# Kernel tuning notes

Hardware: AMD Instinct MI355X
Metric: run time of the kernel (lower is better)

The kernel has to match this reference:

```python
import jax, jax.numpy as jnp
import numpy as np

B, N, H, E, M = 2, 20000, 256, 160000, 512


def setup_inputs() -> dict:
    key = jax.random.key(0)
    ks = jax.random.split(key, 8)
    s = 0.02  # small init scale like trained nets
    return {
        "h": jax.random.normal(ks[0], (B, N, H), jnp.float32),
        "edge_index": jax.random.randint(ks[1], (2, E), 0, N, jnp.int64),
        "msg_w1": jax.random.normal(ks[2], (2 * H, M), jnp.float32) * s,
        "msg_b1": jnp.zeros((M,), jnp.float32),
        "msg_w2": jax.random.normal(ks[3], (M, H), jnp.float32) * s,
        "msg_b2": jnp.zeros((H,), jnp.float32),
        "upd_w1": jax.random.normal(ks[4], (2 * H, M), jnp.float32) * s,
        "upd_b1": jnp.zeros((M,), jnp.float32),
        "upd_w2": jax.random.normal(ks[5], (M, H), jnp.float32) * s,
        "upd_b2": jnp.zeros((H,), jnp.float32),
    }


def _mlp(x, w1, b1, w2, b2):
    return jax.nn.relu(x @ w1 + b1) @ w2 + b2


def reference(h, edge_index, msg_w1, msg_b1, msg_w2, msg_b2,
              upd_w1, upd_b1, upd_w2, upd_b2):
    src, dst = edge_index[0], edge_index[1]
    h_src = h[:, src, :]                         # [B,E,H] gather
    h_dst = h[:, dst, :]                         # [B,E,H] gather
    m = _mlp(jnp.concatenate([h_src, h_dst], axis=-1),
             msg_w1, msg_b1, msg_w2, msg_b2)     # [B,E,H]
    agg = jnp.zeros_like(h).at[:, dst, :].add(m) # scatter-add over dst
    upd = _mlp(jnp.concatenate([h, agg], axis=-1),
               upd_w1, upd_b1, upd_w2, upd_b2)   # [B,N,H]
    return h + upd  # mp_residual=True
```

## Files before the change

### kernel.cpp

```cpp
#include <hip/hip_runtime.h>
#include <hip/hip_bf16.h>
#include <stdint.h>

#define B_ 2
#define N_ 20000
#define H_ 256
#define E_ 160000
#define M_ 512

typedef short bf16x8 __attribute__((ext_vector_type(8)));
typedef float f32x4 __attribute__((ext_vector_type(4)));

__device__ __forceinline__ unsigned short f2bf(float f) {
    union { float f; unsigned u; } cv; cv.f = f;
    unsigned u = cv.u;
    unsigned r = u + 0x7fffu + ((u >> 16) & 1u);
    return (unsigned short)(r >> 16);
}
__device__ __forceinline__ unsigned pack2(float a, float b) {
    return (unsigned)f2bf(a) | ((unsigned)f2bf(b) << 16);
}
__device__ __forceinline__ float bflo(unsigned p) {
    union { unsigned u; float f; } c; c.u = p << 16; return c.f;
}
__device__ __forceinline__ float bfhi(unsigned p) {
    union { unsigned u; float f; } c; c.u = p & 0xffff0000u; return c.f;
}

__global__ void conv_t(const float* __restrict__ W, unsigned short* __restrict__ Wt,
                       int K, int Ncol) {
    int total = Ncol * (K >> 3);
    for (int idx = blockIdx.x * blockDim.x + threadIdx.x; idx < total;
         idx += gridDim.x * blockDim.x) {
        int n = idx % Ncol;
        int kc = (idx / Ncol) << 3;
        unsigned short t[8];
#pragma unroll
        for (int j = 0; j < 8; ++j) t[j] = f2bf(W[(size_t)(kc + j) * Ncol + n]);
        uint4 v;
        v.x = (unsigned)t[0] | ((unsigned)t[1] << 16);
        v.y = (unsigned)t[2] | ((unsigned)t[3] << 16);
        v.z = (unsigned)t[4] | ((unsigned)t[5] << 16);
        v.w = (unsigned)t[6] | ((unsigned)t[7] << 16);
        *(uint4*)(Wt + (size_t)n * K + kc) = v;
    }
}

__global__ void conv_w1pq(const float* __restrict__ W, unsigned short* __restrict__ Wt) {
    int total = 1024 * 32;
    for (int idx = blockIdx.x * blockDim.x + threadIdx.x; idx < total;
         idx += gridDim.x * blockDim.x) {
        int jj = idx & 1023;
        int kc = (idx >> 10) << 3;
        int koff = (jj >= 512) ? 256 : 0;
        int j = jj & 511;
        unsigned short t[8];
#pragma unroll
        for (int r = 0; r < 8; ++r) t[r] = f2bf(W[(size_t)(kc + r + koff) * 512 + j]);
        uint4 v;
        v.x = (unsigned)t[0] | ((unsigned)t[1] << 16);
        v.y = (unsigned)t[2] | ((unsigned)t[3] << 16);
        v.z = (unsigned)t[4] | ((unsigned)t[5] << 16);
        v.w = (unsigned)t[6] | ((unsigned)t[7] << 16);
        *(uint4*)(Wt + (size_t)jj * 256 + kc) = v;
    }
}

__global__ void hist_kernel(const int* __restrict__ eidx, int* __restrict__ cnt) {
    for (int e = blockIdx.x * blockDim.x + threadIdx.x; e < E_;
         e += gridDim.x * blockDim.x)
        atomicAdd(cnt + eidx[E_ + e], 1);
}

__global__ void scan_kernel(const int* __restrict__ cnt, int* __restrict__ offs,
                            int* __restrict__ cursor) {
    __shared__ int part[1024];
    int t = threadIdx.x;
    int base_i = t * 20;
    int loc[20];
    int s = 0;
#pragma unroll 20
    for (int i = 0; i < 20; ++i) {
        int idx = base_i + i;
        int v = (idx < N_) ? cnt[idx] : 0;
        loc[i] = s;
        s += v;
    }
    part[t] = s;
    __syncthreads();
    for (int off = 1; off < 1024; off <<= 1) {
        int tmp = (t >= off) ? part[t - off] : 0;
        __syncthreads();
        if (t >= off) part[t] += tmp;
        __syncthreads();
    }
    int base = part[t] - s;
#pragma unroll 20
    for (int i = 0; i < 20; ++i) {
        int idx = base_i + i;
        if (idx < N_) {
            int o = base + loc[i];
            offs[idx] = o;
            cursor[idx] = o;
        }
    }
    if (t == 1023) offs[N_] = part[1023];
}

__global__ void scatter_kernel(const int* __restrict__ eidx, int* __restrict__ cursor,
                               int* __restrict__ sorted) {
    for (int e = blockIdx.x * blockDim.x + threadIdx.x; e < E_;
         e += gridDim.x * blockDim.x) {
        int d = eidx[E_ + e];
        int pos = atomicAdd(cursor + d, 1);
        sorted[pos] = e;
    }
}

__global__ __launch_bounds__(512, 4) void pq_gemm(
    const float* __restrict__ hb,
    const unsigned short* __restrict__ W1pq,
    unsigned short* __restrict__ PQ) {
    __shared__ char smem[32 * 512];
    const int tid = threadIdx.x;
    const int row0 = blockIdx.x * 32;

#pragma unroll
    for (int it = 0; it < 4; ++it) {
        int linear = it * 512 + tid;
        int row = linear >> 6;
        int c4 = linear & 63;
        float4 v = *(const float4*)(hb + (size_t)(row0 + row) * H_ + c4 * 4);
        int byte = (row * 512 + c4 * 8) ^ ((row & 7) << 4);
        uint2 p;
        p.x = pack2(v.x, v.y);
        p.y = pack2(v.z, v.w);
        *(uint2*)(smem + byte) = p;
    }
    __syncthreads();

    const int lane = tid & 63;
    const int w = tid >> 6;
    const int lo = lane & 15;
    const int hi = lane >> 4;

    f32x4 acc[2][8];
#pragma unroll
    for (int i = 0; i < 2; ++i)
#pragma unroll
        for (int j = 0; j < 8; ++j) acc[i][j] = (f32x4){0.f, 0.f, 0.f, 0.f};

    for (int ks = 0; ks < 256; ks += 32) {
        bf16x8 af[2];
#pragma unroll
        for (int rf = 0; rf < 2; ++rf) {
            int row = rf * 16 + lo;
            int byte = (row * 512 + (ks + 8 * hi) * 2) ^ ((row & 7) << 4);
            af[rf] = *(const bf16x8*)(smem + byte);
        }
#pragma unroll
        for (int cf = 0; cf < 8; ++cf) {
            int col = w * 128 + cf * 16 + lo;
            bf16x8 bfr = *(const bf16x8*)(W1pq + (size_t)col * 256 + ks + 8 * hi);
#pragma unroll
            for (int rf = 0; rf < 2; ++rf)
                acc[rf][cf] = __builtin_amdgcn_mfma_f32_16x16x32_bf16(af[rf], bfr, acc[rf][cf], 0, 0, 0);
        }
    }

#pragma unroll
    for (int cf = 0; cf < 8; ++cf) {
        int col = w * 128 + cf * 16 + lo;
#pragma unroll
        for (int rf = 0; rf < 2; ++rf) {
#pragma unroll
            for (int r = 0; r < 4; ++r) {
                int row = rf * 16 + hi * 4 + r;
                PQ[(size_t)(row0 + row) * 1024 + col] = f2bf(acc[rf][cf][r]);
            }
        }
    }
}

__global__ __launch_bounds__(512, 4) void agg_kernel(
    const unsigned short* __restrict__ PQ,
    const int* __restrict__ eidx,
    const int* __restrict__ sorted,
    const int* __restrict__ offs,
    const int* __restrict__ cnt,
    const unsigned short* __restrict__ w2t,
    const float* __restrict__ b1,
    const float* __restrict__ b2,
    unsigned short* __restrict__ aggb) {
    __shared__ char smem[32 * 1024];
    const int tid = threadIdx.x;
    const int d0 = blockIdx.x * 32;
    const int dsub = tid >> 4;
    const int part = tid & 15;
    const int c0 = part * 32;
    const int d = d0 + dsub;

    unsigned qb[16];
    {
        const unsigned short* qrow = PQ + (size_t)d * 1024 + 512 + c0;
#pragma unroll
        for (int c = 0; c < 4; ++c) {
            bf16x8 qv = *(const bf16x8*)(qrow + c * 8);
#pragma unroll
            for (int jp = 0; jp < 4; ++jp) {
                float q0 = bflo((unsigned)(unsigned short)qv[jp * 2]) + b1[c0 + c * 8 + jp * 2];
                float q1 = bflo((unsigned)(unsigned short)qv[jp * 2 + 1]) + b1[c0 + c * 8 + jp * 2 + 1];
                qb[c * 4 + jp] = pack2(q0, q1);
            }
        }
    }

    float acc[32];
#pragma unroll
    for (int i = 0; i < 32; ++i) acc[i] = 0.f;

    const int beg = offs[d];
    const int end = beg + cnt[d];
    for (int p = beg; p < end; ++p) {
        int e = sorted[p];
        int src = eidx[e];
        const unsigned short* prow = PQ + (size_t)src * 1024 + c0;
#pragma unroll
        for (int c = 0; c < 4; ++c) {
            bf16x8 pv = *(const bf16x8*)(prow + c * 8);
#pragma unroll
            for (int jp = 0; jp < 4; ++jp) {
                unsigned q = qb[c * 4 + jp];
                float p0 = bflo((unsigned)(unsigned short)pv[jp * 2]);
                float p1 = bflo((unsigned)(unsigned short)pv[jp * 2 + 1]);
                acc[c * 8 + jp * 2]     += fmaxf(p0 + bflo(q), 0.f);
                acc[c * 8 + jp * 2 + 1] += fmaxf(p1 + bfhi(q), 0.f);
            }
        }
    }

#pragma unroll
    for (int c = 0; c < 4; ++c) {
        uint4 v;
        v.x = pack2(acc[c * 8 + 0], acc[c * 8 + 1]);
        v.y = pack2(acc[c * 8 + 2], acc[c * 8 + 3]);
        v.z = pack2(acc[c * 8 + 4], acc[c * 8 + 5]);
        v.w = pack2(acc[c * 8 + 6], acc[c * 8 + 7]);
        int byte = (dsub * 1024 + (c0 + c * 8) * 2) ^ ((dsub & 7) << 4);
        *(uint4*)(smem + byte) = v;
    }
    __syncthreads();

    const int lane = tid & 63;
    const int w = tid >> 6;
    const int lo = lane & 15;
    const int hi = lane >> 4;

    f32x4 acc2[2][2];
#pragma unroll
    for (int i = 0; i < 2; ++i)
#pragma unroll
        for (int j = 0; j < 2; ++j) acc2[i][j] = (f32x4){0.f, 0.f, 0.f, 0.f};

    for (int ks = 0; ks < 512; ks += 32) {
        bf16x8 af[2];
#pragma unroll
        for (int rf = 0; rf < 2; ++rf) {
            int row = rf * 16 + lo;
            int byte = (row * 1024 + (ks + 8 * hi) * 2) ^ ((row & 7) << 4);
            af[rf] = *(const bf16x8*)(smem + byte);
        }
#pragma unroll
        for (int cf = 0; cf < 2; ++cf) {
            int col = w * 32 + cf * 16 + lo;
            bf16x8 bfr = *(const bf16x8*)(w2t + (size_t)col * 512 + ks + 8 * hi);
#pragma unroll
            for (int rf = 0; rf < 2; ++rf)
                acc2[rf][cf] = __builtin_amdgcn_mfma_f32_16x16x32_bf16(af[rf], bfr, acc2[rf][cf], 0, 0, 0);
        }
    }

#pragma unroll
    for (int cf = 0; cf < 2; ++cf) {
        int col = w * 32 + cf * 16 + lo;
        float bb = b2[col];
#pragma unroll
        for (int rf = 0; rf < 2; ++rf) {
#pragma unroll
            for (int r = 0; r < 4; ++r) {
                int row = rf * 16 + hi * 4 + r;
                float degf = (float)cnt[d0 + row];
                float v = acc2[rf][cf][r] + degf * bb;
                aggb[(size_t)(d0 + row) * 256 + col] = f2bf(v);
            }
        }
    }
}

__global__ __launch_bounds__(256, 4) void upd_kernel(
    const float* __restrict__ h,
    const unsigned short* __restrict__ aggb,
    const unsigned short* __restrict__ u1t,
    const float* __restrict__ b1,
    const unsigned short* __restrict__ u2t,
    const float* __restrict__ b2,
    float* __restrict__ outp) {
    __shared__ char smem[32 * 1024];
    const int tid = threadIdx.x;
    const int row0 = blockIdx.x * 32;

#pragma unroll
    for (int it = 0; it < 8; ++it) {
        int linear = it * 256 + tid;
        int row = linear >> 6;
        int c8 = linear & 63;
        int grow = row0 + row;
        uint4 v;
        if (c8 < 32) {
            const float* src = h + (size_t)grow * H_ + c8 * 8;
            float4 a = *(const float4*)src;
            float4 b = *(const float4*)(src + 4);
            v.x = pack2(a.x, a.y);
            v.y = pack2(a.z, a.w);
            v.z = pack2(b.x, b.y);
            v.w = pack2(b.z, b.w);
        } else {
            v = *(const uint4*)(aggb + (size_t)grow * 256 + (c8 - 32) * 8);
        }
        int byte = (row * 1024 + c8 * 16) ^ ((row & 7) << 4);
        *(uint4*)(smem + byte) = v;
    }
    __syncthreads();

    const int lane = tid & 63;
    const int w = tid >> 6;
    const int lo = lane & 15;
    const int hi = lane >> 4;

    f32x4 acc[2][8];
#pragma unroll
    for (int i = 0; i < 2; ++i)
#pragma unroll
        for (int j = 0; j < 8; ++j) acc[i][j] = (f32x4){0.f, 0.f, 0.f, 0.f};

    for (int ks = 0; ks < 512; ks += 32) {
        bf16x8 af[2];
#pragma unroll
        for (int rf = 0; rf < 2; ++rf) {
            int row = rf * 16 + lo;
            int byte = (row * 1024 + (ks + 8 * hi) * 2) ^ ((row & 7) << 4);
            af[rf] = *(const bf16x8*)(smem + byte);
        }
#pragma unroll
        for (int cf = 0; cf < 8; ++cf) {
            int col = w * 128 + cf * 16 + lo;
            bf16x8 bfr = *(const bf16x8*)(u1t + (size_t)col * 512 + ks + 8 * hi);
#pragma unroll
            for (int rf = 0; rf < 2; ++rf)
                acc[rf][cf] = __builtin_amdgcn_mfma_f32_16x16x32_bf16(af[rf], bfr, acc[rf][cf], 0, 0, 0);
        }
    }
    __syncthreads();

#pragma unroll
    for (int cf = 0; cf < 8; ++cf) {
        int col = w * 128 + cf * 16 + lo;
        float bb = b1[col];
#pragma unroll
        for (int rf = 0; rf < 2; ++rf) {
#pragma unroll
            for (int r = 0; r < 4; ++r) {
                float v = fmaxf(acc[rf][cf][r] + bb, 0.f);
                int row = rf * 16 + hi * 4 + r;
                int byte = (row * 1024 + col * 2) ^ ((row & 7) << 4);
                *(unsigned short*)(smem + byte) = f2bf(v);
            }
        }
    }
    __syncthreads();

    f32x4 acc2[2][4];
#pragma unroll
    for (int i = 0; i < 2; ++i)
#pragma unroll
        for (int j = 0; j < 4; ++j) acc2[i][j] = (f32x4){0.f, 0.f, 0.f, 0.f};

    for (int ks = 0; ks < 512; ks += 32) {
        bf16x8 af[2];
#pragma unroll
        for (int rf = 0; rf < 2; ++rf) {
            int row = rf * 16 + lo;
            int byte = (row * 1024 + (ks + 8 * hi) * 2) ^ ((row & 7) << 4);
            af[rf] = *(const bf16x8*)(smem + byte);
        }
#pragma unroll
        for (int cf = 0; cf < 4; ++cf) {
            int col = w * 64 + cf * 16 + lo;
            bf16x8 bfr = *(const bf16x8*)(u2t + (size_t)col * 512 + ks + 8 * hi);
#pragma unroll
            for (int rf = 0; rf < 2; ++rf)
                acc2[rf][cf] = __builtin_amdgcn_mfma_f32_16x16x32_bf16(af[rf], bfr, acc2[rf][cf], 0, 0, 0);
        }
    }

#pragma unroll
    for (int cf = 0; cf < 4; ++cf) {
        int col = w * 64 + cf * 16 + lo;
        float bb = b2[col];
#pragma unroll
        for (int rf = 0; rf < 2; ++rf) {
#pragma unroll
            for (int r = 0; r < 4; ++r) {
                int row = rf * 16 + hi * 4 + r;
                size_t o = (size_t)(row0 + row) * H_ + col;
                outp[o] = h[o] + acc2[rf][cf][r] + bb;
            }
        }
    }
}

extern "C" void kernel_launch(void* const* d_in, const int* in_sizes, int n_in,
                              void* d_out, int out_size, void* d_ws, size_t ws_size,
                              hipStream_t stream) {
    const float* h      = (const float*)d_in[0];
    const int*   eidx   = (const int*)d_in[1];
    const float* msg_w1 = (const float*)d_in[2];
    const float* msg_b1 = (const float*)d_in[3];
    const float* msg_w2 = (const float*)d_in[4];
    const float* msg_b2 = (const float*)d_in[5];
    const float* upd_w1 = (const float*)d_in[6];
    const float* upd_b1 = (const float*)d_in[7];
    const float* upd_w2 = (const float*)d_in[8];
    const float* upd_b2 = (const float*)d_in[9];
    float* out = (float*)d_out;

    char* ws = (char*)d_ws;
    size_t off = 0;
    auto alloc = [&](size_t bytes) {
        char* p = ws + off;
        off = (off + bytes + 255) & ~(size_t)255;
        return p;
    };
    unsigned short* PQ    = (unsigned short*)alloc((size_t)N_ * 1024 * 2);
    unsigned short* aggb  = (unsigned short*)alloc((size_t)B_ * N_ * 256 * 2);
    unsigned short* w1pq  = (unsigned short*)alloc(1024 * 256 * 2);
    unsigned short* w2t   = (unsigned short*)alloc(256 * 512 * 2);
    unsigned short* u1t   = (unsigned short*)alloc(512 * 512 * 2);
    unsigned short* u2t   = (unsigned short*)alloc(256 * 512 * 2);
    int* cnt    = (int*)alloc(N_ * 4);
    int* offs   = (int*)alloc((N_ + 1) * 4);
    int* cursor = (int*)alloc(N_ * 4);
    int* sorted = (int*)alloc(E_ * 4);
    if (ws_size < off) return;

    hipMemsetAsync(cnt, 0, N_ * 4, stream);
    conv_w1pq<<<64, 256, 0, stream>>>(msg_w1, w1pq);
    conv_t<<<64, 256, 0, stream>>>(msg_w2, w2t, 512, 256);
    conv_t<<<128, 256, 0, stream>>>(upd_w1, u1t, 512, 512);
    conv_t<<<64, 256, 0, stream>>>(upd_w2, u2t, 512, 256);

    hist_kernel<<<256, 256, 0, stream>>>(eidx, cnt);
    scan_kernel<<<1, 1024, 0, stream>>>(cnt, offs, cursor);
    scatter_kernel<<<256, 256, 0, stream>>>(eidx, cursor, sorted);

    for (int b = 0; b < B_; ++b) {
        pq_gemm<<<N_ / 32, 512, 0, stream>>>(h + (size_t)b * N_ * H_, w1pq, PQ);
        agg_kernel<<<N_ / 32, 512, 0, stream>>>(PQ, eidx, sorted, offs, cnt, w2t,
                                                msg_b1, msg_b2,
                                                aggb + (size_t)b * N_ * 256);
    }

    upd_kernel<<<(B_ * N_) / 32, 256, 0, stream>>>(h, aggb, u1t, upd_b1, u2t, upd_b2, out);
}
```

Before: 487.3 us.

## Enlarge GEMM tiles, prefetch weights, store src ids directly, interleave agg columns

Several changes land together. The four weight-conversion launches become one kernel, and the CSR array now stores source node ids so the agg loop skips one indirection. The agg loop handles two edges per iteration with an interleaved column layout so gather loads coalesce across lanes. The pq_gemm and upd_kernel tiles grow to 64 rows (upd now runs 512 threads), and all MFMA loops register-prefetch the next B fragment. Larger tiles and prefetch buffers raise register and LDS pressure and may lower occupancy.

```diff
diff --git a/kernel.cpp b/kernel.cpp
--- a/kernel.cpp
+++ b/kernel.cpp
@@ -27,42 +27,52 @@
     union { unsigned u; float f; } c; c.u = p & 0xffff0000u; return c.f;
 }
 
-__global__ void conv_t(const float* __restrict__ W, unsigned short* __restrict__ Wt,
-                       int K, int Ncol) {
-    int total = Ncol * (K >> 3);
-    for (int idx = blockIdx.x * blockDim.x + threadIdx.x; idx < total;
-         idx += gridDim.x * blockDim.x) {
-        int n = idx % Ncol;
-        int kc = (idx / Ncol) << 3;
-        unsigned short t[8];
-#pragma unroll
-        for (int j = 0; j < 8; ++j) t[j] = f2bf(W[(size_t)(kc + j) * Ncol + n]);
-        uint4 v;
-        v.x = (unsigned)t[0] | ((unsigned)t[1] << 16);
-        v.y = (unsigned)t[2] | ((unsigned)t[3] << 16);
-        v.z = (unsigned)t[4] | ((unsigned)t[5] << 16);
-        v.w = (unsigned)t[6] | ((unsigned)t[7] << 16);
-        *(uint4*)(Wt + (size_t)n * K + kc) = v;
-    }
-}
-
-__global__ void conv_w1pq(const float* __restrict__ W, unsigned short* __restrict__ Wt) {
-    int total = 1024 * 32;
-    for (int idx = blockIdx.x * blockDim.x + threadIdx.x; idx < total;
-         idx += gridDim.x * blockDim.x) {
-        int jj = idx & 1023;
-        int kc = (idx >> 10) << 3;
-        int koff = (jj >= 512) ? 256 : 0;
-        int j = jj & 511;
-        unsigned short t[8];
-#pragma unroll
-        for (int r = 0; r < 8; ++r) t[r] = f2bf(W[(size_t)(kc + r + koff) * 512 + j]);
-        uint4 v;
-        v.x = (unsigned)t[0] | ((unsigned)t[1] << 16);
-        v.y = (unsigned)t[2] | ((unsigned)t[3] << 16);
-        v.z = (unsigned)t[4] | ((unsigned)t[5] << 16);
-        v.w = (unsigned)t[6] | ((unsigned)t[7] << 16);
-        *(uint4*)(Wt + (size_t)jj * 256 + kc) = v;
+__device__ __forceinline__ void conv_t_one(const float* __restrict__ W,
+                                           unsigned short* __restrict__ Wt,
+                                           int K, int Ncol, int idx) {
+    int n = idx % Ncol;
+    int kc = (idx / Ncol) << 3;
+    unsigned short t[8];
+#pragma unroll
+    for (int j = 0; j < 8; ++j) t[j] = f2bf(W[(size_t)(kc + j) * Ncol + n]);
+    uint4 v;
+    v.x = (unsigned)t[0] | ((unsigned)t[1] << 16);
+    v.y = (unsigned)t[2] | ((unsigned)t[3] << 16);
+    v.z = (unsigned)t[4] | ((unsigned)t[5] << 16);
+    v.w = (unsigned)t[6] | ((unsigned)t[7] << 16);
+    *(uint4*)(Wt + (size_t)n * K + kc) = v;
+}
+
+__device__ __forceinline__ void conv_w1pq_one(const float* __restrict__ W,
+                                              unsigned short* __restrict__ Wt, int idx) {
+    int jj = idx & 1023;
+    int kc = (idx >> 10) << 3;
+    int koff = (jj >= 512) ? 256 : 0;
+    int j = jj & 511;
+    unsigned short t[8];
+#pragma unroll
+    for (int r = 0; r < 8; ++r) t[r] = f2bf(W[(size_t)(kc + r + koff) * 512 + j]);
+    uint4 v;
+    v.x = (unsigned)t[0] | ((unsigned)t[1] << 16);
+    v.y = (unsigned)t[2] | ((unsigned)t[3] << 16);
+    v.z = (unsigned)t[4] | ((unsigned)t[5] << 16);
+    v.w = (unsigned)t[6] | ((unsigned)t[7] << 16);
+    *(uint4*)(Wt + (size_t)jj * 256 + kc) = v;
+}
+
+__global__ void conv_all(const float* __restrict__ mw1, const float* __restrict__ mw2,
+                         const float* __restrict__ uw1, const float* __restrict__ uw2,
+                         unsigned short* __restrict__ w1pq, unsigned short* __restrict__ w2t,
+                         unsigned short* __restrict__ u1t, unsigned short* __restrict__ u2t) {
+    int idx = blockIdx.x * blockDim.x + threadIdx.x;
+    if (idx < 32768) {
+        conv_w1pq_one(mw1, w1pq, idx);
+    } else if (idx < 32768 + 16384) {
+        conv_t_one(mw2, w2t, 512, 256, idx - 32768);
+    } else if (idx < 32768 + 16384 + 32768) {
+        conv_t_one(uw1, u1t, 512, 512, idx - (32768 + 16384));
+    } else if (idx < 98304) {
+        conv_t_one(uw2, u2t, 512, 256, idx - (32768 + 16384 + 32768));
     }
 }
 
@@ -108,12 +118,12 @@
 }
 
 __global__ void scatter_kernel(const int* __restrict__ eidx, int* __restrict__ cursor,
-                               int* __restrict__ sorted) {
+                               int* __restrict__ srcs) {
     for (int e = blockIdx.x * blockDim.x + threadIdx.x; e < E_;
          e += gridDim.x * blockDim.x) {
         int d = eidx[E_ + e];
         int pos = atomicAdd(cursor + d, 1);
-        sorted[pos] = e;
+        srcs[pos] = eidx[e];
     }
 }
 
@@ -121,16 +131,18 @@
     const float* __restrict__ hb,
     const unsigned short* __restrict__ W1pq,
     unsigned short* __restrict__ PQ) {
-    __shared__ char smem[32 * 512];
+    __shared__ char smem[64 * 512];
     const int tid = threadIdx.x;
-    const int row0 = blockIdx.x * 32;
-
-#pragma unroll
-    for (int it = 0; it < 4; ++it) {
+    const int row0 = blockIdx.x * 64;
+
+#pragma unroll
+    for (int it = 0; it < 8; ++it) {
         int linear = it * 512 + tid;
         int row = linear >> 6;
         int c4 = linear & 63;
-        float4 v = *(const float4*)(hb + (size_t)(row0 + row) * H_ + c4 * 4);
+        int grow = row0 + row;
+        if (grow >= N_) grow = N_ - 1;
+        float4 v = *(const float4*)(hb + (size_t)grow * H_ + c4 * 4);
         int byte = (row * 512 + c4 * 8) ^ ((row & 7) << 4);
         uint2 p;
         p.x = pack2(v.x, v.y);
@@ -143,40 +155,55 @@
     const int w = tid >> 6;
     const int lo = lane & 15;
     const int hi = lane >> 4;
-
-    f32x4 acc[2][8];
-#pragma unroll
-    for (int i = 0; i < 2; ++i)
+    const int colw = w * 128;
+
+    f32x4 acc[4][8];
+#pragma unroll
+    for (int i = 0; i < 4; ++i)
 #pragma unroll
         for (int j = 0; j < 8; ++j) acc[i][j] = (f32x4){0.f, 0.f, 0.f, 0.f};
 
+    bf16x8 bcur[8];
+#pragma unroll
+    for (int cf = 0; cf < 8; ++cf)
+        bcur[cf] = *(const bf16x8*)(W1pq + (size_t)(colw + cf * 16 + lo) * 256 + 8 * hi);
+
+#pragma unroll
     for (int ks = 0; ks < 256; ks += 32) {
-        bf16x8 af[2];
-#pragma unroll
-        for (int rf = 0; rf < 2; ++rf) {
+        bf16x8 bnx[8];
+        if (ks + 32 < 256) {
+#pragma unroll
+            for (int cf = 0; cf < 8; ++cf)
+                bnx[cf] = *(const bf16x8*)(W1pq + (size_t)(colw + cf * 16 + lo) * 256 + ks + 32 + 8 * hi);
+        }
+        bf16x8 af[4];
+#pragma unroll
+        for (int rf = 0; rf < 4; ++rf) {
             int row = rf * 16 + lo;
             int byte = (row * 512 + (ks + 8 * hi) * 2) ^ ((row & 7) << 4);
             af[rf] = *(const bf16x8*)(smem + byte);
         }
 #pragma unroll
-        for (int cf = 0; cf < 8; ++cf) {
-            int col = w * 128 + cf * 16 + lo;
-            bf16x8 bfr = *(const bf16x8*)(W1pq + (size_t)col * 256 + ks + 8 * hi);
-#pragma unroll
-            for (int rf = 0; rf < 2; ++rf)
-                acc[rf][cf] = __builtin_amdgcn_mfma_f32_16x16x32_bf16(af[rf], bfr, acc[rf][cf], 0, 0, 0);
+        for (int cf = 0; cf < 8; ++cf)
+#pragma unroll
+            for (int rf = 0; rf < 4; ++rf)
+                acc[rf][cf] = __builtin_amdgcn_mfma_f32_16x16x32_bf16(af[rf], bcur[cf], acc[rf][cf], 0, 0, 0);
+        if (ks + 32 < 256) {
+#pragma unroll
+            for (int cf = 0; cf < 8; ++cf) bcur[cf] = bnx[cf];
         }
     }
 
 #pragma unroll
     for (int cf = 0; cf < 8; ++cf) {
-        int col = w * 128 + cf * 16 + lo;
-#pragma unroll
-        for (int rf = 0; rf < 2; ++rf) {
+        int col = colw + cf * 16 + lo;
+#pragma unroll
+        for (int rf = 0; rf < 4; ++rf) {
 #pragma unroll
             for (int r = 0; r < 4; ++r) {
                 int row = rf * 16 + hi * 4 + r;
-                PQ[(size_t)(row0 + row) * 1024 + col] = f2bf(acc[rf][cf][r]);
+                if (row0 + row < N_)
+                    PQ[(size_t)(row0 + row) * 1024 + col] = f2bf(acc[rf][cf][r]);
             }
         }
     }
@@ -184,8 +211,7 @@
 
 __global__ __launch_bounds__(512, 4) void agg_kernel(
     const unsigned short* __restrict__ PQ,
-    const int* __restrict__ eidx,
-    const int* __restrict__ sorted,
+    const int* __restrict__ srcs,
     const int* __restrict__ offs,
     const int* __restrict__ cnt,
     const unsigned short* __restrict__ w2t,
@@ -197,19 +223,19 @@
     const int d0 = blockIdx.x * 32;
     const int dsub = tid >> 4;
     const int part = tid & 15;
-    const int c0 = part * 32;
     const int d = d0 + dsub;
 
     unsigned qb[16];
     {
-        const unsigned short* qrow = PQ + (size_t)d * 1024 + 512 + c0;
+        const unsigned short* qrow = PQ + (size_t)d * 1024 + 512;
 #pragma unroll
         for (int c = 0; c < 4; ++c) {
-            bf16x8 qv = *(const bf16x8*)(qrow + c * 8);
+            int cb = (c * 16 + part) * 8;
+            bf16x8 qv = *(const bf16x8*)(qrow + cb);
 #pragma unroll
             for (int jp = 0; jp < 4; ++jp) {
-                float q0 = bflo((unsigned)(unsigned short)qv[jp * 2]) + b1[c0 + c * 8 + jp * 2];
-                float q1 = bflo((unsigned)(unsigned short)qv[jp * 2 + 1]) + b1[c0 + c * 8 + jp * 2 + 1];
+                float q0 = bflo((unsigned)(unsigned short)qv[jp * 2]) + b1[cb + jp * 2];
+                float q1 = bflo((unsigned)(unsigned short)qv[jp * 2 + 1]) + b1[cb + jp * 2 + 1];
                 qb[c * 4 + jp] = pack2(q0, q1);
             }
         }
@@ -220,21 +246,43 @@
     for (int i = 0; i < 32; ++i) acc[i] = 0.f;
 
     const int beg = offs[d];
-    const int end = beg + cnt[d];
-    for (int p = beg; p < end; ++p) {
-        int e = sorted[p];
-        int src = eidx[e];
-        const unsigned short* prow = PQ + (size_t)src * 1024 + c0;
+    const int end = offs[d + 1];
+    int p = beg;
+    for (; p + 1 < end; p += 2) {
+        int s0 = srcs[p];
+        int s1 = srcs[p + 1];
+        const unsigned short* r0 = PQ + (size_t)s0 * 1024;
+        const unsigned short* r1 = PQ + (size_t)s1 * 1024;
+        bf16x8 v0[4], v1[4];
 #pragma unroll
         for (int c = 0; c < 4; ++c) {
-            bf16x8 pv = *(const bf16x8*)(prow + c * 8);
+            v0[c] = *(const bf16x8*)(r0 + (c * 16 + part) * 8);
+            v1[c] = *(const bf16x8*)(r1 + (c * 16 + part) * 8);
+        }
+#pragma unroll
+        for (int c = 0; c < 4; ++c) {
 #pragma unroll
             for (int jp = 0; jp < 4; ++jp) {
                 unsigned q = qb[c * 4 + jp];
-                float p0 = bflo((unsigned)(unsigned short)pv[jp * 2]);
-                float p1 = bflo((unsigned)(unsigned short)pv[jp * 2 + 1]);
-                acc[c * 8 + jp * 2]     += fmaxf(p0 + bflo(q), 0.f);
-                acc[c * 8 + jp * 2 + 1] += fmaxf(p1 + bfhi(q), 0.f);
+                float ql = bflo(q), qh = bfhi(q);
+                acc[c * 8 + jp * 2] += fmaxf(bflo((unsigned)(unsigned short)v0[c][jp * 2]) + ql, 0.f)
+                                     + fmaxf(bflo((unsigned)(unsigned short)v1[c][jp * 2]) + ql, 0.f);
+                acc[c * 8 + jp * 2 + 1] += fmaxf(bflo((unsigned)(unsigned short)v0[c][jp * 2 + 1]) + qh, 0.f)
+                                         + fmaxf(bflo((unsigned)(unsigned short)v1[c][jp * 2 + 1]) + qh, 0.f);
+            }
+        }
+    }
+    if (p < end) {
+        int s0 = srcs[p];
+        const unsigned short* r0 = PQ + (size_t)s0 * 1024;
+#pragma unroll
+        for (int c = 0; c < 4; ++c) {
+            bf16x8 v0 = *(const bf16x8*)(r0 + (c * 16 + part) * 8);
+#pragma unroll
+            for (int jp = 0; jp < 4; ++jp) {
+                unsigned q = qb[c * 4 + jp];
+                acc[c * 8 + jp * 2]     += fmaxf(bflo((unsigned)(unsigned short)v0[jp * 2]) + bflo(q), 0.f);
+                acc[c * 8 + jp * 2 + 1] += fmaxf(bflo((unsigned)(unsigned short)v0[jp * 2 + 1]) + bfhi(q), 0.f);
             }
         }
     }
@@ -246,7 +294,7 @@
         v.y = pack2(acc[c * 8 + 2], acc[c * 8 + 3]);
         v.z = pack2(acc[c * 8 + 4], acc[c * 8 + 5]);
         v.w = pack2(acc[c * 8 + 6], acc[c * 8 + 7]);
-        int byte = (dsub * 1024 + (c0 + c * 8) * 2) ^ ((dsub & 7) << 4);
+        int byte = (dsub * 1024 + (c * 16 + part) * 16) ^ ((dsub & 7) << 4);
         *(uint4*)(smem + byte) = v;
     }
     __syncthreads();
@@ -255,6 +303,7 @@
     const int w = tid >> 6;
     const int lo = lane & 15;
     const int hi = lane >> 4;
+    const int colw = w * 32;
 
     f32x4 acc2[2][2];
 #pragma unroll
@@ -262,7 +311,19 @@
 #pragma unroll
         for (int j = 0; j < 2; ++j) acc2[i][j] = (f32x4){0.f, 0.f, 0.f, 0.f};
 
+    bf16x8 bcur[2];
+#pragma unroll
+    for (int cf = 0; cf < 2; ++cf)
+        bcur[cf] = *(const bf16x8*)(w2t + (size_t)(colw + cf * 16 + lo) * 512 + 8 * hi);
+
+#pragma unroll
     for (int ks = 0; ks < 512; ks += 32) {
+        bf16x8 bnx[2];
+        if (ks + 32 < 512) {
+#pragma unroll
+            for (int cf = 0; cf < 2; ++cf)
+                bnx[cf] = *(const bf16x8*)(w2t + (size_t)(colw + cf * 16 + lo) * 512 + ks + 32 + 8 * hi);
+        }
         bf16x8 af[2];
 #pragma unroll
         for (int rf = 0; rf < 2; ++rf) {
@@ -271,18 +332,19 @@
             af[rf] = *(const bf16x8*)(smem + byte);
         }
 #pragma unroll
-        for (int cf = 0; cf < 2; ++cf) {
-            int col = w * 32 + cf * 16 + lo;
-            bf16x8 bfr = *(const bf16x8*)(w2t + (size_t)col * 512 + ks + 8 * hi);
+        for (int cf = 0; cf < 2; ++cf)
 #pragma unroll
             for (int rf = 0; rf < 2; ++rf)
-                acc2[rf][cf] = __builtin_amdgcn_mfma_f32_16x16x32_bf16(af[rf], bfr, acc2[rf][cf], 0, 0, 0);
+                acc2[rf][cf] = __builtin_amdgcn_mfma_f32_16x16x32_bf16(af[rf], bcur[cf], acc2[rf][cf], 0, 0, 0);
+        if (ks + 32 < 512) {
+#pragma unroll
+            for (int cf = 0; cf < 2; ++cf) bcur[cf] = bnx[cf];
         }
     }
 
 #pragma unroll
     for (int cf = 0; cf < 2; ++cf) {
-        int col = w * 32 + cf * 16 + lo;
+        int col = colw + cf * 16 + lo;
         float bb = b2[col];
 #pragma unroll
         for (int rf = 0; rf < 2; ++rf) {
@@ -290,14 +352,13 @@
             for (int r = 0; r < 4; ++r) {
                 int row = rf * 16 + hi * 4 + r;
                 float degf = (float)cnt[d0 + row];
-                float v = acc2[rf][cf][r] + degf * bb;
-                aggb[(size_t)(d0 + row) * 256 + col] = f2bf(v);
-            }
-        }
-    }
-}
-
-__global__ __launch_bounds__(256, 4) void upd_kernel(
+                aggb[(size_t)(d0 + row) * 256 + col] = f2bf(acc2[rf][cf][r] + degf * bb);
+            }
+        }
+    }
+}
+
+__global__ __launch_bounds__(512, 4) void upd_kernel(
     const float* __restrict__ h,
     const unsigned short* __restrict__ aggb,
     const unsigned short* __restrict__ u1t,
@@ -305,13 +366,13 @@
     const unsigned short* __restrict__ u2t,
     const float* __restrict__ b2,
     float* __restrict__ outp) {
-    __shared__ char smem[32 * 1024];
+    __shared__ char smem[64 * 1024];
     const int tid = threadIdx.x;
-    const int row0 = blockIdx.x * 32;
+    const int row0 = blockIdx.x * 64;
 
 #pragma unroll
     for (int it = 0; it < 8; ++it) {
-        int linear = it * 256 + tid;
+        int linear = it * 512 + tid;
         int row = linear >> 6;
         int c8 = linear & 63;
         int grow = row0 + row;
@@ -337,83 +398,115 @@
     const int lo = lane & 15;
     const int hi = lane >> 4;
 
-    f32x4 acc[2][8];
-#pragma unroll
-    for (int i = 0; i < 2; ++i)
-#pragma unroll
-        for (int j = 0; j < 8; ++j) acc[i][j] = (f32x4){0.f, 0.f, 0.f, 0.f};
-
-    for (int ks = 0; ks < 512; ks += 32) {
-        bf16x8 af[2];
-#pragma unroll
-        for (int rf = 0; rf < 2; ++rf) {
-            int row = rf * 16 + lo;
-            int byte = (row * 1024 + (ks + 8 * hi) * 2) ^ ((row & 7) << 4);
-            af[rf] = *(const bf16x8*)(smem + byte);
-        }
-#pragma unroll
-        for (int cf = 0; cf < 8; ++cf) {
-            int col = w * 128 + cf * 16 + lo;
-            bf16x8 bfr = *(const bf16x8*)(u1t + (size_t)col * 512 + ks + 8 * hi);
-#pragma unroll
-            for (int rf = 0; rf < 2; ++rf)
-                acc[rf][cf] = __builtin_amdgcn_mfma_f32_16x16x32_bf16(af[rf], bfr, acc[rf][cf], 0, 0, 0);
+    {
+        const int colw = w * 64;
+        f32x4 acc[4][4];
+#pragma unroll
+        for (int i = 0; i < 4; ++i)
+#pragma unroll
+            for (int j = 0; j < 4; ++j) acc[i][j] = (f32x4){0.f, 0.f, 0.f, 0.f};
+
+        bf16x8 bcur[4];
+#pragma unroll
+        for (int cf = 0; cf < 4; ++cf)
+            bcur[cf] = *(const bf16x8*)(u1t + (size_t)(colw + cf * 16 + lo) * 512 + 8 * hi);
+
+#pragma unroll
+        for (int ks = 0; ks < 512; ks += 32) {
+            bf16x8 bnx[4];
+            if (ks + 32 < 512) {
+#pragma unroll
+                for (int cf = 0; cf < 4; ++cf)
+                    bnx[cf] = *(const bf16x8*)(u1t + (size_t)(colw + cf * 16 + lo) * 512 + ks + 32 + 8 * hi);
+            }
+            bf16x8 af[4];
+#pragma unroll
+            for (int rf = 0; rf < 4; ++rf) {
+                int row = rf * 16 + lo;
+                int byte = (row * 1024 + (ks + 8 * hi) * 2) ^ ((row & 7) << 4);
+                af[rf] = *(const bf16x8*)(smem + byte);
+            }
+#pragma unroll
+            for (int cf = 0; cf < 4; ++cf)
+#pragma unroll
+                for (int rf = 0; rf < 4; ++rf)
+                    acc[rf][cf] = __builtin_amdgcn_mfma_f32_16x16x32_bf16(af[rf], bcur[cf], acc[rf][cf], 0, 0, 0);
+            if (ks + 32 < 512) {
+#pragma unroll
+                for (int cf = 0; cf < 4; ++cf) bcur[cf] = bnx[cf];
+            }
+        }
+        __syncthreads();
+
+#pragma unroll
+        for (int cf = 0; cf < 4; ++cf) {
+            int col = colw + cf * 16 + lo;
+            float bb = b1[col];
+#pragma unroll
+            for (int rf = 0; rf < 4; ++rf) {
+#pragma unroll
+                for (int r = 0; r < 4; ++r) {
+                    float v = fmaxf(acc[rf][cf][r] + bb, 0.f);
+                    int row = rf * 16 + hi * 4 + r;
+                    int byte = (row * 1024 + col * 2) ^ ((row & 7) << 4);
+                    *(unsigned short*)(smem + byte) = f2bf(v);
+                }
+            }
         }
     }
     __syncthreads();
 
-#pragma unroll
-    for (int cf = 0; cf < 8; ++cf) {
-        int col = w * 128 + cf * 16 + lo;
-        float bb = b1[col];
-#pragma unroll
-        for (int rf = 0; rf < 2; ++rf) {
-#pragma unroll
-            for (int r = 0; r < 4; ++r) {
-                float v = fmaxf(acc[rf][cf][r] + bb, 0.f);
-                int row = rf * 16 + hi * 4 + r;
-                int byte = (row * 1024 + col * 2) ^ ((row & 7) << 4);
-                *(unsigned short*)(smem + byte) = f2bf(v);
-            }
-        }
-    }
-    __syncthreads();
-
-    f32x4 acc2[2][4];
-#pragma unroll
-    for (int i = 0; i < 2; ++i)
-#pragma unroll
-        for (int j = 0; j < 4; ++j) acc2[i][j] = (f32x4){0.f, 0.f, 0.f, 0.f};
-
-    for (int ks = 0; ks < 512; ks += 32) {
-        bf16x8 af[2];
-#pragma unroll
-        for (int rf = 0; rf < 2; ++rf) {
-            int row = rf * 16 + lo;
-            int byte = (row * 1024 + (ks + 8 * hi) * 2) ^ ((row & 7) << 4);
-            af[rf] = *(const bf16x8*)(smem + byte);
-        }
-#pragma unroll
-        for (int cf = 0; cf < 4; ++cf) {
-            int col = w * 64 + cf * 16 + lo;
-            bf16x8 bfr = *(const bf16x8*)(u2t + (size_t)col * 512 + ks + 8 * hi);
-#pragma unroll
-            for (int rf = 0; rf < 2; ++rf)
-                acc2[rf][cf] = __builtin_amdgcn_mfma_f32_16x16x32_bf16(af[rf], bfr, acc2[rf][cf], 0, 0, 0);
-        }
-    }
-
-#pragma unroll
-    for (int cf = 0; cf < 4; ++cf) {
-        int col = w * 64 + cf * 16 + lo;
-        float bb = b2[col];
-#pragma unroll
-        for (int rf = 0; rf < 2; ++rf) {
-#pragma unroll
-            for (int r = 0; r < 4; ++r) {
-                int row = rf * 16 + hi * 4 + r;
-                size_t o = (size_t)(row0 + row) * H_ + col;
-                outp[o] = h[o] + acc2[rf][cf][r] + bb;
+    {
+        const int colw = w * 32;
+        f32x4 acc2[4][2];
+#pragma unroll
+        for (int i = 0; i < 4; ++i)
+#pragma unroll
+            for (int j = 0; j < 2; ++j) acc2[i][j] = (f32x4){0.f, 0.f, 0.f, 0.f};
+
+        bf16x8 bcur[2];
+#pragma unroll
+        for (int cf = 0; cf < 2; ++cf)
+            bcur[cf] = *(const bf16x8*)(u2t + (size_t)(colw + cf * 16 + lo) * 512 + 8 * hi);
+
+#pragma unroll
+        for (int ks = 0; ks < 512; ks += 32) {
+            bf16x8 bnx[2];
+            if (ks + 32 < 512) {
+#pragma unroll
+                for (int cf = 0; cf < 2; ++cf)
+                    bnx[cf] = *(const bf16x8*)(u2t + (size_t)(colw + cf * 16 + lo) * 512 + ks + 32 + 8 * hi);
+            }
+            bf16x8 af[4];
+#pragma unroll
+            for (int rf = 0; rf < 4; ++rf) {
+                int row = rf * 16 + lo;
+                int byte = (row * 1024 + (ks + 8 * hi) * 2) ^ ((row & 7) << 4);
+                af[rf] = *(const bf16x8*)(smem + byte);
+            }
+#pragma unroll
+            for (int cf = 0; cf < 2; ++cf)
+#pragma unroll
+                for (int rf = 0; rf < 4; ++rf)
+                    acc2[rf][cf] = __builtin_amdgcn_mfma_f32_16x16x32_bf16(af[rf], bcur[cf], acc2[rf][cf], 0, 0, 0);
+            if (ks + 32 < 512) {
+#pragma unroll
+                for (int cf = 0; cf < 2; ++cf) bcur[cf] = bnx[cf];
+            }
+        }
+
+#pragma unroll
+        for (int cf = 0; cf < 2; ++cf) {
+            int col = colw + cf * 16 + lo;
+            float bb = b2[col];
+#pragma unroll
+            for (int rf = 0; rf < 4; ++rf) {
+#pragma unroll
+                for (int r = 0; r < 4; ++r) {
+                    int row = rf * 16 + hi * 4 + r;
+                    size_t o = (size_t)(row0 + row) * H_ + col;
+                    outp[o] = h[o] + acc2[rf][cf][r] + bb;
+                }
             }
         }
     }
@@ -441,34 +534,31 @@
         off = (off + bytes + 255) & ~(size_t)255;
         return p;
     };
-    unsigned short* PQ    = (unsigned short*)alloc((size_t)N_ * 1024 * 2);
-    unsigned short* aggb  = (unsigned short*)alloc((size_t)B_ * N_ * 256 * 2);
-    unsigned short* w1pq  = (unsigned short*)alloc(1024 * 256 * 2);
-    unsigned short* w2t   = (unsigned short*)alloc(256 * 512 * 2);
-    unsigned short* u1t   = (unsigned short*)alloc(512 * 512 * 2);
-    unsigned short* u2t   = (unsigned short*)alloc(256 * 512 * 2);
+    unsigned short* PQ   = (unsigned short*)alloc((size_t)N_ * 1024 * 2);
+    unsigned short* aggb = (unsigned short*)alloc((size_t)B_ * N_ * 256 * 2);
+    unsigned short* w1pq = (unsigned short*)alloc(1024 * 256 * 2);
+    unsigned short* w2t  = (unsigned short*)alloc(256 * 512 * 2);
+    unsigned short* u1t  = (unsigned short*)alloc(512 * 512 * 2);
+    unsigned short* u2t  = (unsigned short*)alloc(256 * 512 * 2);
     int* cnt    = (int*)alloc(N_ * 4);
     int* offs   = (int*)alloc((N_ + 1) * 4);
     int* cursor = (int*)alloc(N_ * 4);
-    int* sorted = (int*)alloc(E_ * 4);
+    int* srcs   = (int*)alloc(E_ * 4);
     if (ws_size < off) return;
 
     hipMemsetAsync(cnt, 0, N_ * 4, stream);
-    conv_w1pq<<<64, 256, 0, stream>>>(msg_w1, w1pq);
-    conv_t<<<64, 256, 0, stream>>>(msg_w2, w2t, 512, 256);
-    conv_t<<<128, 256, 0, stream>>>(upd_w1, u1t, 512, 512);
-    conv_t<<<64, 256, 0, stream>>>(upd_w2, u2t, 512, 256);
+    conv_all<<<384, 256, 0, stream>>>(msg_w1, msg_w2, upd_w1, upd_w2, w1pq, w2t, u1t, u2t);
 
     hist_kernel<<<256, 256, 0, stream>>>(eidx, cnt);
     scan_kernel<<<1, 1024, 0, stream>>>(cnt, offs, cursor);
-    scatter_kernel<<<256, 256, 0, stream>>>(eidx, cursor, sorted);
+    scatter_kernel<<<256, 256, 0, stream>>>(eidx, cursor, srcs);
 
     for (int b = 0; b < B_; ++b) {
-        pq_gemm<<<N_ / 32, 512, 0, stream>>>(h + (size_t)b * N_ * H_, w1pq, PQ);
-        agg_kernel<<<N_ / 32, 512, 0, stream>>>(PQ, eidx, sorted, offs, cnt, w2t,
+        pq_gemm<<<(N_ + 63) / 64, 512, 0, stream>>>(h + (size_t)b * N_ * H_, w1pq, PQ);
+        agg_kernel<<<N_ / 32, 512, 0, stream>>>(PQ, srcs, offs, cnt, w2t,
                                                 msg_b1, msg_b2,
                                                 aggb + (size_t)b * N_ * 256);
     }
 
-    upd_kernel<<<(B_ * N_) / 32, 256, 0, stream>>>(h, aggb, u1t, upd_b1, u2t, upd_b2, out);
-}
+    upd_kernel<<<(B_ * N_) / 64, 512, 0, stream>>>(h, aggb, u1t, upd_b1, u2t, upd_b2, out);
+}
```

After: 596.0 us. +22.3%, slower.
